# Optimization experiments

Measured on AMD Instinct MI355X. Metric: run time of the kernel, lower is better.

## Reference

```python
import jax, jax.numpy as jnp
import numpy as np

B, C, H, NH = 4, 512, 768, 12        # docs, seq len, hidden, attn heads
NE, MM = 20, 23                      # entities/doc, max mentions/entity
NP_ = NE * (NE - 1)                  # 380 head-tail pairs per doc
QS, POS, EMB, BLK, NB = 128, 128, 768, 64, 12
NCLS = 97
NEG = -10000.0

def _lin(k, i, o):
    return jax.random.normal(k, (i, o), jnp.float32) / np.sqrt(i)

def setup_inputs():
    key = jax.random.key(0)
    ks = jax.random.split(key, 24)
    seq = jax.random.normal(ks[0], (B, C, H), jnp.float32)
    att = jax.random.uniform(ks[1], (B, NH, C, C), jnp.float32)
    midx = jax.random.randint(ks[2], (B, NE, MM), 0, C)
    cnt = jax.random.randint(ks[3], (B, NE), 1, MM + 1)
    mmask = (jnp.arange(MM)[None, None, :] < cnt[:, :, None]).astype(jnp.float32)
    hh, tt = jnp.meshgrid(jnp.arange(NE), jnp.arange(NE), indexing='ij')
    off = ~jnp.eye(NE, dtype=bool)
    hts = jnp.stack([hh[off], tt[off]], -1)
    hts = jnp.broadcast_to(hts[None], (B, NP_, 2))
    vis = (jax.random.uniform(ks[4], (B, NP_, NP_)) > 0.3).astype(jnp.float32)
    inp = dict(sequence_output=seq, attention=att, mention_idx=midx,
               mention_mask=mmask, hts=hts, visible_mask=vis)
    wspec = [('Wcq', H, QS), ('Weq', H, QS), ('Whe', 2 * H, EMB), ('Wte', 2 * H, EMB),
             ('Wbl', EMB * BLK, EMB), ('Wpp', EMB + 2 * POS, EMB),
             ('Wgq', EMB, EMB), ('Wgk', EMB, EMB), ('Wgv', EMB, EMB),
             ('Wp1', 3 * EMB, EMB), ('Wp2', EMB, NCLS)]
    for j, (nm, i, o) in enumerate(wspec):
        inp[nm] = _lin(ks[5 + j], i, o)
        inp['b' + nm[1:]] = jnp.zeros((o,), jnp.float32)
    for nm in ('bgq', 'bgk', 'bgv'):
        inp.pop(nm)
    inp['pos_emb'] = jax.random.normal(ks[20], (42, POS), jnp.float32) * 0.02
    return inp

def reference(sequence_output, attention, mention_idx, mention_mask, hts, visible_mask,
              Wcq, bcq, Weq, beq, Whe, bhe, Wte, bte, Wbl, bbl, Wpp, bpp,
              Wgq, Wgk, Wgv, Wp1, bp1, Wp2, bp2, pos_emb):
    b3 = jnp.arange(B)[:, None, None]
    # per-entity mention gather (padded mentions zeroed, as in the torch loop)
    ent_emb = sequence_output[b3, mention_idx] * mention_mask[..., None]        # [B,NE,MM,H]
    att_t = jnp.transpose(attention, (0, 2, 1, 3))                              # [B,C,NH,C]
    ent_att = att_t[b3, mention_idx] * mention_mask[..., None, None]            # [B,NE,MM,NH,C]
    cnt = mention_mask.sum(-1)[..., None, None]
    ent_att = ent_att.sum(2) / cnt                                              # mean over valid mentions [B,NE,NH,C]

    bi = jnp.arange(B)[:, None]
    hi, ti = hts[..., 0], hts[..., 1]
    hs_m, ts_m = ent_emb[bi, hi], ent_emb[bi, ti]                               # [B,P,MM,H]
    hmask, tmask = mention_mask[bi, hi], mention_mask[bi, ti]                   # [B,P,MM]
    ht_att = (ent_att[bi, hi] * ent_att[bi, ti]).mean(2)                        # mean over heads [B,P,C]
    ht_att = ht_att / (ht_att.sum(-1, keepdims=True) + 1e-5)
    rs = jnp.einsum('bld,bpl->bpd', sequence_output, ht_att)                    # context [B,P,H]

    htq = rs @ Wcq + bcq                                                        # [B,P,QS]
    scale = 1.0 / np.sqrt(EMB)                                                  # original divides by sqrt(emb_size)
    G1 = jnp.einsum('bpq,bpmq->bpm', htq, hs_m @ Weq + beq) * scale
    G2 = jnp.einsum('bpq,bpmq->bpm', htq, ts_m @ Weq + beq) * scale
    G1 = jnp.where(hmask > 0, G1, NEG)
    G2 = jnp.where(tmask > 0, G2, NEG)
    hs = jnp.einsum('bpm,bpmh->bph', jax.nn.softmax(G1, -1), hs_m)
    ts = jnp.einsum('bpm,bpmh->bph', jax.nn.softmax(G2, -1), ts_m)

    hs = jnp.tanh(jnp.concatenate([hs, rs], -1) @ Whe + bhe)                    # [B,P,EMB]
    ts = jnp.tanh(jnp.concatenate([ts, rs], -1) @ Wte + bte)
    bh = hs.reshape(B, NP_, NB, BLK)
    bt = ts.reshape(B, NP_, NB, BLK)
    pair = (bh[..., :, None] * bt[..., None, :]).reshape(B, NP_, EMB * BLK)     # grouped bilinear feature
    pair = pair @ Wbl + bbl                                                     # [B,P,EMB]
    hs_core, ts_core = pos_emb[hi], pos_emb[ti]                                 # [B,P,POS]
    pair = jnp.tanh(jnp.concatenate([hs_core, pair, ts_core], -1) @ Wpp + bpp)

    # pair graph: one masked self-attention layer over pairs with residual
    q, k, v = pair @ Wgq, pair @ Wgk, pair @ Wgv
    sc = jnp.einsum('bpd,bqd->bpq', q, k) / np.sqrt(EMB)
    sc = jnp.where(visible_mask > 0, sc, NEG)
    pair = pair + jnp.einsum('bpq,bqd->bpd', jax.nn.softmax(sc, -1), v)

    feat = jnp.concatenate([hs, ts, pair], -1)                                  # [B,P,3*EMB]
    logits = jnp.tanh(feat @ Wp1 + bp1) @ Wp2 + bp2                             # dropout is identity at eval
    return logits.reshape(B * NP_, NCLS)
```

## Files before the change

### kernel.cpp

```cpp
#include <hip/hip_runtime.h>
#include <hip/hip_bf16.h>

#define Bn   4
#define Cn   512
#define Hn   768
#define NHn  12
#define NEn  20
#define MMn  23
#define Pn   380
#define Mr   1520
#define QSn  128
#define NEGV (-10000.0f)
#define SCL  0.036084391824351615f

typedef unsigned int uint32;
typedef __attribute__((ext_vector_type(4))) float float4v;
typedef __attribute__((ext_vector_type(2))) _Float16 half2v;
typedef __attribute__((ext_vector_type(2))) __fp16 fp16x2;
typedef __attribute__((ext_vector_type(8))) _Float16 half8;

__device__ __forceinline__ unsigned short f2h(float f){
    return __builtin_bit_cast(unsigned short, (_Float16)f);
}
__device__ __forceinline__ uint32 pkrtz(float a, float b){
    fp16x2 h = __builtin_amdgcn_cvt_pkrtz(a, b);
    return __builtin_bit_cast(uint32, h);
}
__device__ __forceinline__ half8 mulsplat(half8 a, uint32 hd){
    half2v s = __builtin_bit_cast(half2v, hd);
    union { half8 h; half2v c[4]; } u, v;
    u.h = a;
    #pragma unroll
    for (int i = 0; i < 4; i++) v.c[i] = u.c[i] * s;
    return v.h;
}
__device__ __forceinline__ void gl_lds16(const unsigned short* g, unsigned short* l){
    __builtin_amdgcn_global_load_lds(
        (const __attribute__((address_space(1))) void*)g,
        (__attribute__((address_space(3))) void*)l, 16, 0, 0);
}

static const size_t o_HS = 0;
static const size_t o_TS = 1167360;
static const size_t o_PB = 2334720;
static const size_t Xo   = 3502080;
static const size_t oEA = Xo;
static const size_t oEE = Xo+491520;
static const size_t oEK = Xo+1904640;
static const size_t oHA = Xo+2140160;
static const size_t oHQ = Xo+2918400;
static const size_t oSH = Xo+3112960;
static const size_t oST = Xo+4280320;
static const size_t oRS = Xo+5447680;
static const size_t oSEQT = Xo+6615040;
static const size_t oWCQ = Xo;
static const size_t oWEQ = Xo+49152;
static const size_t oWHE = Xo;
static const size_t oWTE = Xo+589824;
static const size_t oWBL = Xo;
static const size_t oFP = Xo;
static const size_t oPT = Xo+1556480;
static const size_t oQ  = Xo+2723840;
static const size_t oKT = Xo+3891200;
static const size_t oV  = Xo+5058560;
static const size_t oP2 = Xo+6225920;
static const size_t oT1 = Xo+7393280;
static const size_t oWPP = Xo+8560640;
static const size_t oWGQ = Xo+8953856;
static const size_t oWGK = Xo+9248768;
static const size_t oWGV = Xo+9543680;
static const size_t oWP1 = Xo+9838592;
static const size_t oWP2 = Xo+10723328;


__global__ __launch_bounds__(256) void k_ent_att(const float* __restrict__ att,
    const int* __restrict__ midx, const float* __restrict__ mmask, float* __restrict__ ea)
{
    int x = blockIdx.x;
    int nh = x % NHn; int e = (x / NHn) % NEn; int b = x / (NHn * NEn);
    __shared__ int   sidx[MMn];
    __shared__ float smsk[MMn];
    int t = threadIdx.x;
    if (t < MMn) { sidx[t] = midx[(b*NEn+e)*MMn + t]; smsk[t] = mmask[(b*NEn+e)*MMn + t]; }
    __syncthreads();
    float cnt = 0.f;
    for (int m = 0; m < MMn; m++) cnt += smsk[m];
    for (int c = t; c < Cn; c += 256) {
        float acc = 0.f;
        for (int m = 0; m < MMn; m++)
            acc += smsk[m] * att[((size_t)(b*NHn+nh)*Cn + sidx[m])*Cn + c];
        ea[(size_t)x*Cn + c] = acc / cnt;
    }
}

__global__ __launch_bounds__(256) void k_ent_emb(const float* __restrict__ seq,
    const int* __restrict__ midx, const float* __restrict__ mmask, float* __restrict__ ee)
{
    int x = blockIdx.x;
    int b = x / (NEn*MMn);
    int idx = midx[x]; float msk = mmask[x];
    int t = threadIdx.x;
    for (int h = t; h < Hn; h += 256)
        ee[(size_t)x*Hn + h] = msk * seq[((size_t)b*Cn + idx)*Hn + h];
}

__global__ __launch_bounds__(256) void k_htatt(const float* __restrict__ ea,
    const int* __restrict__ hts, float* __restrict__ hta)
{
    int row = blockIdx.x; int b = row / Pn;
    int he = hts[row*2], te = hts[row*2+1];
    __shared__ float sc[Cn];
    __shared__ float red[256];
    int t = threadIdx.x;
    const float* eah = ea + (size_t)(b*NEn+he)*NHn*Cn;
    const float* eat = ea + (size_t)(b*NEn+te)*NHn*Cn;
    for (int c = t; c < Cn; c += 256) {
        float a = 0.f;
        for (int nh = 0; nh < NHn; nh++) a += eah[nh*Cn+c]*eat[nh*Cn+c];
        sc[c] = a * (1.0f/NHn);
    }
    __syncthreads();
    float ps = sc[t] + sc[t+256];
    red[t] = ps; __syncthreads();
    for (int s = 128; s > 0; s >>= 1) { if (t < s) red[t] += red[t+s]; __syncthreads(); }
    float inv = 1.0f/(red[0] + 1e-5f);
    for (int c = t; c < Cn; c += 256) hta[(size_t)row*Cn + c] = sc[c]*inv;
}

__global__ __launch_bounds__(256) void k_select(const float* __restrict__ htq,
    const float* __restrict__ ekey, const float* __restrict__ ee,
    const float* __restrict__ mmask, const int* __restrict__ hts,
    float* __restrict__ selh, float* __restrict__ selt)
{
    int row = blockIdx.x; int side = blockIdx.y;
    int b = row / Pn;
    int e = hts[row*2 + side];
    __shared__ float qv[QSn];
    __shared__ float gsc[MMn];
    __shared__ float ew[MMn];
    int t = threadIdx.x;
    if (t < QSn) qv[t] = htq[(size_t)row*QSn + t];
    __syncthreads();
    if (t < MMn) {
        const float* kr = ekey + ((size_t)(b*NEn+e)*MMn + t)*QSn;
        float g = 0.f;
        for (int qq = 0; qq < QSn; qq++) g += qv[qq]*kr[qq];
        g *= SCL;
        float msk = mmask[(b*NEn+e)*MMn + t];
        gsc[t] = (msk > 0.f) ? g : NEGV;
    }
    __syncthreads();
    float mx = -1e30f;
    for (int m = 0; m < MMn; m++) mx = fmaxf(mx, gsc[m]);
    if (t < MMn) ew[t] = expf(gsc[t] - mx);
    __syncthreads();
    float s = 0.f;
    for (int m = 0; m < MMn; m++) s += ew[m];
    float invs = 1.0f/s;
    float* dst = side ? selt : selh;
    const float* eb = ee + (size_t)(b*NEn+e)*MMn*Hn;
    for (int h = t; h < Hn; h += 256) {
        float o = 0.f;
        for (int m = 0; m < MMn; m++) o += ew[m]*eb[(size_t)m*Hn + h];
        dst[(size_t)row*Hn + h] = o*invs;
    }
}

struct WD { const float* src; unsigned short* dst; int K; int N; int Npad; int t0; };
struct WT8 { WD d[8]; int nd; };

__global__ __launch_bounds__(256) void k_wtr(WT8 tab)
{
    int b = blockIdx.x;
    int i = 0;
    while (i+1 < tab.nd && b >= tab.d[i+1].t0) i++;
    WD d = tab.d[i];
    int tile = b - d.t0;
    int ktiles = d.K >> 6;
    int kt = tile % ktiles, nt = tile / ktiles;
    int k0 = kt*64, n0 = nt*64;
    __shared__ __align__(16) unsigned short tl[64][72];
    int t = threadIdx.x;
    int nl = t & 63, rq = t >> 6;
    #pragma unroll
    for (int r = 0; r < 16; r++) {
        int kl = r*4 + rq;
        float v = (n0+nl < d.N) ? d.src[(size_t)(k0+kl)*d.N + n0 + nl] : 0.f;
        tl[nl][kl] = f2h(v);
    }
    __syncthreads();
    int nn2 = t >> 2, kk0 = (t & 3) * 16;
    uint4 a = *(const uint4*)&tl[nn2][kk0];
    uint4 bq = *(const uint4*)&tl[nn2][kk0+8];
    uint4* dst = (uint4*)&d.dst[(size_t)(n0+nn2)*d.K + k0 + kk0];
    dst[0] = a; dst[1] = bq;
}

template<int MODE, int TM>
__global__ __launch_bounds__(256,4) void k_gmfma(
    const float* __restrict__ A0, const float* __restrict__ A1, const float* __restrict__ A2,
    int KA, int KB, int KC,
    const unsigned short* __restrict__ Wt,
    const float* __restrict__ bias, float* __restrict__ out,
    float* __restrict__ out2, float* __restrict__ out3,
    int Mtot, int N, int kchunk,
    long aStride, long wStride, long oStride)
{
    __shared__ __align__(16) unsigned short sa[64][72];
    __shared__ __align__(16) unsigned short sw[64][72];
    int t = threadIdx.x;
    int K = KA + KB + KC;
    int row0 = blockIdx.x * 64;
    int n0 = blockIdx.y * 64;
    int bz = blockIdx.z;
    const float* Ab = A0; const unsigned short* W = Wt; float* O = out;
    if (MODE & 32) { Ab += (size_t)bz*aStride; W += (size_t)bz*wStride; O += (size_t)bz*oStride; }
    int k0 = 0, k1 = K;
    if (MODE & 1) { k0 = bz*kchunk; k1 = k0 + kchunk; }
    int lane = t & 63, w = t >> 6, ln = lane & 15, q = lane >> 4;
    int sr = t >> 2;
    int sk = (t & 3) * 16;
    int rA = row0 + sr; if (rA > Mtot-1) rA = Mtot-1;

    float4v acc[4];
    #pragma unroll
    for (int mt = 0; mt < 4; mt++) acc[mt] = (float4v)0.f;

    for (int kk = k0; kk < k1; kk += 64) {
        const float* src; int kloc, Kl, seg;
        if (kk < KA)            { src = Ab; kloc = kk;          Kl = KA; seg = 0; }
        else if (kk < KA + KB)  { src = A1; kloc = kk - KA;     Kl = KB; seg = 1; }
        else                    { src = A2; kloc = kk - KA - KB; Kl = KC; seg = 2; }
        const float* ap = &src[(size_t)rA*Kl + kloc + sk];
        float4 v0 = ((const float4*)ap)[0];
        float4 v1 = ((const float4*)ap)[1];
        float4 v2 = ((const float4*)ap)[2];
        float4 v3 = ((const float4*)ap)[3];
        if (TM && ((TM >> seg) & 1)) {
            v0.x = tanhf(v0.x); v0.y = tanhf(v0.y); v0.z = tanhf(v0.z); v0.w = tanhf(v0.w);
            v1.x = tanhf(v1.x); v1.y = tanhf(v1.y); v1.z = tanhf(v1.z); v1.w = tanhf(v1.w);
            v2.x = tanhf(v2.x); v2.y = tanhf(v2.y); v2.z = tanhf(v2.z); v2.w = tanhf(v2.w);
            v3.x = tanhf(v3.x); v3.y = tanhf(v3.y); v3.z = tanhf(v3.z); v3.w = tanhf(v3.w);
        }
        const uint4* gw = (const uint4*)&W[(size_t)(n0+sr)*K + kk + sk];
        uint4 w0 = gw[0], w1 = gw[1];
        uint4 pa, pb;
        pa.x = pkrtz(v0.x, v0.y); pa.y = pkrtz(v0.z, v0.w);
        pa.z = pkrtz(v1.x, v1.y); pa.w = pkrtz(v1.z, v1.w);
        pb.x = pkrtz(v2.x, v2.y); pb.y = pkrtz(v2.z, v2.w);
        pb.z = pkrtz(v3.x, v3.y); pb.w = pkrtz(v3.z, v3.w);
        *(uint4*)&sa[sr][sk]   = pa;
        *(uint4*)&sa[sr][sk+8] = pb;
        *(uint4*)&sw[sr][sk]   = w0;
        *(uint4*)&sw[sr][sk+8] = w1;
        __syncthreads();
        half8 b0 = *(const half8*)&sw[w*16+ln][q*8];
        half8 b1 = *(const half8*)&sw[w*16+ln][32 + q*8];
        #pragma unroll
        for (int mt = 0; mt < 4; mt++) {
            half8 a0 = *(const half8*)&sa[mt*16+ln][q*8];
            half8 a1 = *(const half8*)&sa[mt*16+ln][32 + q*8];
            acc[mt] = __builtin_amdgcn_mfma_f32_16x16x32_f16(a0, b0, acc[mt], 0, 0, 0);
            acc[mt] = __builtin_amdgcn_mfma_f32_16x16x32_f16(a1, b1, acc[mt], 0, 0, 0);
        }
        __syncthreads();
    }
    int nn = n0 + w*16 + ln;
    if (MODE & 16) {
        int sg = nn / Hn; int nl = nn - sg*Hn;
        #pragma unroll
        for (int mt = 0; mt < 4; mt++) {
            #pragma unroll
            for (int r = 0; r < 4; r++) {
                int row = row0 + mt*16 + q*4 + r;
                if (row >= Mtot) continue;
                float val = acc[mt][r];
                if (sg == 0)      out [(size_t)row*Hn + nl] = val;
                else if (sg == 2) out3[(size_t)row*Hn + nl] = val;
                else {
                    int bb = row / Pn, pp = row % Pn;
                    out2[((size_t)bb*Hn + nl)*Pn + pp] = val;
                }
            }
        }
        return;
    }
    if (nn >= N) return;
    float bv = (MODE & 4) ? bias[nn] : 0.f;
    #pragma unroll
    for (int mt = 0; mt < 4; mt++) {
        #pragma unroll
        for (int r = 0; r < 4; r++) {
            int row = row0 + mt*16 + q*4 + r;
            if (row >= Mtot) continue;
            float val = acc[mt][r];
            if (MODE & 1) atomicAdd(&O[(size_t)row*N + nn], val);
            else          O[(size_t)row*N + nn] = val + bv;
        }
    }
}

__global__ __launch_bounds__(256) void k_binit(const float* __restrict__ bias,
    float* __restrict__ o, int N)
{
    int idx = blockIdx.x*256 + threadIdx.x;
    o[idx] = bias[idx % N];
}

__global__ __launch_bounds__(256) void k_binit3(const float* __restrict__ b0,
    const float* __restrict__ b1, const float* __restrict__ b2, float* __restrict__ o)
{
    int idx = blockIdx.x*256 + threadIdx.x;
    int r = idx / (Mr*Hn);
    const float* bb = (r == 0) ? b0 : ((r == 1) ? b1 : b2);
    o[idx] = bb[idx % Hn];
}

__global__ __launch_bounds__(256,3) void k_blmfma(const float* __restrict__ hs,
    const float* __restrict__ ts, const unsigned short* __restrict__ Wt,
    float* __restrict__ pb)
{
    __shared__ __align__(16) unsigned short hsl[2][64][64];
    __shared__ __align__(16) unsigned short tsl[2][64][64];
    __shared__ __align__(16) unsigned short wbuf[2][64][64];
    int t = threadIdx.x;
    int bid = blockIdx.x + 24*(blockIdx.y + 12*(int)blockIdx.z);
    int sb = (bid & 7)*216 + (bid >> 3);
    int p_t = sb % 24; int r2 = sb / 24;
    int p0 = p_t * 64;
    int d0 = (r2 % 12) * 64;
    int g  = r2 / 12;
    int lane = t & 63, w = t >> 6, ln = lane & 15, q = lane >> 4;
    int xr = (ln & 7) << 3;

    const unsigned short* Wd = Wt + (size_t)d0*49152;
    auto stage = [&](int cc, int bufi){
        int n2 = 2*g + (cc >> 6);
        size_t kb = (size_t)n2*4096 + (size_t)(cc & 63)*64;
        #pragma unroll
        for (int pass = 0; pass < 2; pass++) {
            int r = pass*32 + (t >> 3);
            int c0s = (t & 7) * 8;
            gl_lds16(Wd + (size_t)r*49152 + kb + (c0s ^ ((r & 7) << 3)),
                     &wbuf[bufi][r][c0s]);
        }
    };
    stage(0, 0);

    {
        int p = t & 63; int s = t >> 6;
        int nn = s >> 1; int c0 = (s & 1) * 32;
        int xw = (p & 7) << 3;
        int pr = p0 + p; if (pr > Mr-1) pr = Mr-1;
        int n = 2*g + nn;
        const float* hp = hs + (size_t)pr*Hn + n*64 + c0;
        const float* tp = ts + (size_t)pr*Hn + n*64 + c0;
        #pragma unroll
        for (int b2 = 0; b2 < 2; b2++) {
            const float4* hp4 = (const float4*)(hp + b2*16);
            const float4* tp4 = (const float4*)(tp + b2*16);
            float4 x0=hp4[0], x1=hp4[1], x2=hp4[2], x3=hp4[3];
            uint4 oh, oh2;
            oh.x = pkrtz(tanhf(x0.x),tanhf(x0.y)); oh.y = pkrtz(tanhf(x0.z),tanhf(x0.w));
            oh.z = pkrtz(tanhf(x1.x),tanhf(x1.y)); oh.w = pkrtz(tanhf(x1.z),tanhf(x1.w));
            oh2.x = pkrtz(tanhf(x2.x),tanhf(x2.y)); oh2.y = pkrtz(tanhf(x2.z),tanhf(x2.w));
            oh2.z = pkrtz(tanhf(x3.x),tanhf(x3.y)); oh2.w = pkrtz(tanhf(x3.z),tanhf(x3.w));
            *(uint4*)&hsl[nn][p][(c0 + b2*16)     ^ xw] = oh;
            *(uint4*)&hsl[nn][p][(c0 + b2*16 + 8) ^ xw] = oh2;
            float4 y0=tp4[0], y1=tp4[1], y2=tp4[2], y3=tp4[3];
            uint4 ot, ot2;
            ot.x = pkrtz(tanhf(y0.x),tanhf(y0.y)); ot.y = pkrtz(tanhf(y0.z),tanhf(y0.w));
            ot.z = pkrtz(tanhf(y1.x),tanhf(y1.y)); ot.w = pkrtz(tanhf(y1.z),tanhf(y1.w));
            ot2.x = pkrtz(tanhf(y2.x),tanhf(y2.y)); ot2.y = pkrtz(tanhf(y2.z),tanhf(y2.w));
            ot2.z = pkrtz(tanhf(y3.x),tanhf(y3.y)); ot2.w = pkrtz(tanhf(y3.z),tanhf(y3.w));
            *(uint4*)&tsl[nn][p][(c0 + b2*16)     ^ xw] = ot;
            *(uint4*)&tsl[nn][p][(c0 + b2*16 + 8) ^ xw] = ot2;
        }
    }
    __syncthreads();

    float4v acc[4];
    #pragma unroll
    for (int e = 0; e < 4; e++) acc[e] = (float4v)0.f;

    int buf = 0;
    #pragma unroll
    for (int nn = 0; nn < 2; nn++) {
        half8 tsr0[4], tsr1[4];
        #pragma unroll
        for (int e = 0; e < 4; e++) {
            tsr0[e] = *(const half8*)&tsl[nn][e*16+ln][(q*8) ^ xr];
            tsr1[e] = *(const half8*)&tsl[nn][e*16+ln][(32 + q*8) ^ xr];
        }
        for (int ci = 0; ci < 64; ci++) {
            int cc = nn*64 + ci;
            if (cc + 1 < 128) stage(cc+1, buf^1);
            uint32 hd[4];
            #pragma unroll
            for (int e = 0; e < 4; e++) {
                uint32 hv = hsl[nn][e*16+ln][ci ^ xr];
                hd[e] = __builtin_amdgcn_perm(hv, hv, 0x01000100u);
            }
            #pragma unroll
            for (int c = 0; c < 2; c++) {
                half8 wf = *(const half8*)&wbuf[buf][w*16+ln][(c*32 + q*8) ^ xr];
                #pragma unroll
                for (int e = 0; e < 4; e++) {
                    half8 bfr = mulsplat(c ? tsr1[e] : tsr0[e], hd[e]);
                    acc[e] = __builtin_amdgcn_mfma_f32_16x16x32_f16(wf, bfr, acc[e], 0, 0, 0);
                }
            }
            __syncthreads();
            buf ^= 1;
        }
    }
    #pragma unroll
    for (int e = 0; e < 4; e++) {
        int p = p0 + e*16 + ln;
        if (p >= Mr) continue;
        int dbase = d0 + w*16 + q*4;
        #pragma unroll
        for (int r = 0; r < 4; r++)
            atomicAdd(&pb[(size_t)p*Hn + dbase + r], acc[e][r]);
    }
}


__global__ __launch_bounds__(256) void k_featpp(const float* __restrict__ pairbl,
    const float* __restrict__ pos, const int* __restrict__ hts, float* __restrict__ fpp)
{
    int row = blockIdx.x; int t = threadIdx.x;
    int he = hts[row*2], te = hts[row*2+1];
    float* dst = fpp + (size_t)row*1024;
    if (t < 128) { dst[t] = pos[he*128 + t]; dst[896 + t] = pos[te*128 + t]; }
    for (int h = t; h < Hn; h += 256) dst[128 + h] = pairbl[(size_t)row*Hn + h];
}

__global__ __launch_bounds__(256) void k_graph(const float* __restrict__ q,
    const float* __restrict__ kT, const float* __restrict__ v, const float* __restrict__ vis,
    const float* __restrict__ pairT, float* __restrict__ pair2)
{
    int row = blockIdx.x; int b = row / Pn; int p = row % Pn;
    __shared__ float qs[Hn];
    __shared__ float sc[Pn];
    __shared__ float red[256];
    int t = threadIdx.x;
    for (int h = t; h < Hn; h += 256) qs[h] = q[(size_t)row*Hn + h];
    __syncthreads();
    for (int qq = t; qq < Pn; qq += 256) {
        const float* kcol = kT + (size_t)b*Hn*Pn + qq;
        float a = 0.f;
        for (int h = 0; h < Hn; h++) a += qs[h]*kcol[(size_t)h*Pn];
        a *= SCL;
        float ms = vis[((size_t)b*Pn + p)*Pn + qq];
        sc[qq] = (ms > 0.f) ? a : NEGV;
    }
    __syncthreads();
    float mx = -1e30f;
    for (int qq = t; qq < Pn; qq += 256) mx = fmaxf(mx, sc[qq]);
    red[t] = mx; __syncthreads();
    for (int s = 128; s > 0; s >>= 1) { if (t < s) red[t] = fmaxf(red[t], red[t+s]); __syncthreads(); }
    mx = red[0];
    __syncthreads();
    float ps = 0.f;
    for (int qq = t; qq < Pn; qq += 256) { float e2 = expf(sc[qq]-mx); sc[qq] = e2; ps += e2; }
    red[t] = ps; __syncthreads();
    for (int s = 128; s > 0; s >>= 1) { if (t < s) red[t] += red[t+s]; __syncthreads(); }
    float invs = 1.0f/red[0];
    __syncthreads();
    float a0 = 0.f, a1 = 0.f, a2 = 0.f;
    for (int qq = 0; qq < Pn; qq++) {
        float sv = sc[qq];
        const float* vr = v + ((size_t)b*Pn+qq)*Hn + t;
        a0 += sv*vr[0]; a1 += sv*vr[256]; a2 += sv*vr[512];
    }
    const float* pt = pairT + (size_t)row*Hn + t;
    float* o = pair2 + (size_t)row*Hn + t;
    o[0]   = tanhf(pt[0])   + a0*invs;
    o[256] = tanhf(pt[256]) + a1*invs;
    o[512] = tanhf(pt[512]) + a2*invs;
}

__global__ __launch_bounds__(256) void k_fillu(unsigned int* p, unsigned int v, int n){
    int i = blockIdx.x*256 + threadIdx.x;
    if (i < n) p[i] = v;
}

extern "C" void kernel_launch(void* const* d_in, const int* in_sizes, int n_in,
                              void* d_out, int out_size, void* d_ws, size_t ws_size,
                              hipStream_t stream)
{
    const float* seq  = (const float*)d_in[0];
    const float* att  = (const float*)d_in[1];
    const int*   midx = (const int*)d_in[2];
    const float* mmask= (const float*)d_in[3];
    const int*   hts  = (const int*)d_in[4];
    const float* vis  = (const float*)d_in[5];
    const float* Wcq = (const float*)d_in[6];  const float* bcq = (const float*)d_in[7];
    const float* Weq = (const float*)d_in[8];  const float* beq = (const float*)d_in[9];
    const float* Whe = (const float*)d_in[10]; const float* bhe = (const float*)d_in[11];
    const float* Wte = (const float*)d_in[12]; const float* bte = (const float*)d_in[13];
    const float* Wbl = (const float*)d_in[14]; const float* bbl = (const float*)d_in[15];
    const float* Wpp = (const float*)d_in[16]; const float* bpp = (const float*)d_in[17];
    const float* Wgq = (const float*)d_in[18];
    const float* Wgk = (const float*)d_in[19];
    const float* Wgv = (const float*)d_in[20];
    const float* Wp1 = (const float*)d_in[21]; const float* bp1 = (const float*)d_in[22];
    const float* Wp2 = (const float*)d_in[23]; const float* bp2 = (const float*)d_in[24];
    const float* pos = (const float*)d_in[25];
    float* ws = (float*)d_ws;
    float* out = (float*)d_out;
    const float* nul = nullptr;
    float* nulw = nullptr;

    if (ws_size < 89505792ULL) {
        int n = out_size/2;
        k_fillu<<<(n+255)/256, 256, 0, stream>>>((unsigned int*)d_out, 0x476A476Au, n);
        return;
    }

    unsigned short* WCQt = (unsigned short*)(ws + oWCQ);
    unsigned short* WEQt = (unsigned short*)(ws + oWEQ);
    unsigned short* SEQt = (unsigned short*)(ws + oSEQT);
    unsigned short* WHEt = (unsigned short*)(ws + oWHE);
    unsigned short* WTEt = (unsigned short*)(ws + oWTE);
    unsigned short* WBLt = (unsigned short*)(ws + oWBL);
    unsigned short* WPPt = (unsigned short*)(ws + oWPP);
    unsigned short* WGQt = (unsigned short*)(ws + oWGQ);
    unsigned short* WP1t = (unsigned short*)(ws + oWP1);
    unsigned short* WP2t = (unsigned short*)(ws + oWP2);

    k_ent_att<<<Bn*NEn*NHn, 256, 0, stream>>>(att, midx, mmask, ws + oEA);
    k_ent_emb<<<Bn*NEn*MMn, 256, 0, stream>>>(seq, midx, mmask, ws + oEE);
    k_htatt<<<Mr, 256, 0, stream>>>(ws + oEA, hts, ws + oHA);

    {
        WT8 tb{}; tb.nd = 6;
        tb.d[0] = { Wcq, WCQt, 768, 128, 128, 0 };
        tb.d[1] = { Weq, WEQt, 768, 128, 128, 24 };
        for (int b = 0; b < 4; b++)
            tb.d[2+b] = { seq + (size_t)b*Cn*Hn, SEQt + (size_t)b*Hn*Cn, Cn, Hn, Hn, 48 + b*96 };
        k_wtr<<<432, 256, 0, stream>>>(tb);
    }
    k_gmfma<32,0><<<dim3(6,12,4), 256, 0, stream>>>(ws + oHA, nul, nul, Cn, 0, 0,
        SEQt, nul, ws + oRS, nulw, nulw, Pn, Hn, 0,
        (long)Pn*Cn, (long)Hn*Cn, (long)Pn*Hn);
    k_gmfma<4,0><<<dim3(24,2,1), 256, 0, stream>>>(ws + oRS, nul, nul, Hn, 0, 0,
        WCQt, bcq, ws + oHQ, nulw, nulw, Mr, QSn, 0, 0, 0, 0);
    k_gmfma<4,0><<<dim3(29,2,1), 256, 0, stream>>>(ws + oEE, nul, nul, Hn, 0, 0,
        WEQt, beq, ws + oEK, nulw, nulw, Bn*NEn*MMn, QSn, 0, 0, 0, 0);
    k_select<<<dim3(Mr,2), 256, 0, stream>>>(ws + oHQ, ws + oEK, ws + oEE,
        mmask, hts, ws + oSH, ws + oST);

    {
        WT8 tb{}; tb.nd = 2;
        tb.d[0] = { Whe, WHEt, 1536, 768, 768, 0 };
        tb.d[1] = { Wte, WTEt, 1536, 768, 768, 288 };
        k_wtr<<<576, 256, 0, stream>>>(tb);
    }
    k_binit3<<<(3*Mr*Hn)/256, 256, 0, stream>>>(bhe, bte, bbl, ws + o_HS);
    k_gmfma<1,0><<<dim3(24,12,3), 256, 0, stream>>>(ws + oSH, ws + oRS, nul, Hn, Hn, 0,
        WHEt, nul, ws + o_HS, nulw, nulw, Mr, Hn, 512, 0, 0, 0);
    k_gmfma<1,0><<<dim3(24,12,3), 256, 0, stream>>>(ws + oST, ws + oRS, nul, Hn, Hn, 0,
        WTEt, nul, ws + o_TS, nulw, nulw, Mr, Hn, 512, 0, 0, 0);

    {
        WT8 tb{}; tb.nd = 1;
        tb.d[0] = { Wbl, WBLt, 49152, 768, 768, 0 };
        k_wtr<<<9216, 256, 0, stream>>>(tb);
    }
    k_blmfma<<<dim3(24,12,6), 256, 0, stream>>>(ws + o_HS, ws + o_TS, WBLt, ws + o_PB);

    k_featpp<<<Mr, 256, 0, stream>>>(ws + o_PB, pos, hts, ws + oFP);

    {
        WT8 tb{}; tb.nd = 6;
        tb.d[0] = { Wpp, WPPt, 1024, 768, 768, 0 };
        tb.d[1] = { Wgq, WGQt, 768, 768, 768, 192 };
        tb.d[2] = { Wgk, (unsigned short*)(ws + oWGK), 768, 768, 768, 336 };
        tb.d[3] = { Wgv, (unsigned short*)(ws + oWGV), 768, 768, 768, 480 };
        tb.d[4] = { Wp1, WP1t, 2304, 768, 768, 624 };
        tb.d[5] = { Wp2, WP2t, 768, 97, 128, 1056 };
        k_wtr<<<1080, 256, 0, stream>>>(tb);
    }
    k_binit<<<(Mr*Hn)/256, 256, 0, stream>>>(bpp, ws + oPT, Hn);
    k_gmfma<1,0><<<dim3(24,12,2), 256, 0, stream>>>(ws + oFP, nul, nul, 1024, 0, 0,
        WPPt, nul, ws + oPT, nulw, nulw, Mr, Hn, 512, 0, 0, 0);
    k_gmfma<16,1><<<dim3(24,36,1), 256, 0, stream>>>(ws + oPT, nul, nul, Hn, 0, 0,
        WGQt, nul, ws + oQ, ws + oKT, ws + oV, Mr, 3*Hn, 0, 0, 0, 0);
    k_graph<<<Mr, 256, 0, stream>>>(ws + oQ, ws + oKT, ws + oV, vis, ws + oPT, ws + oP2);
    k_binit<<<(Mr*Hn)/256, 256, 0, stream>>>(bp1, ws + oT1, Hn);
    k_gmfma<1,3><<<dim3(24,12,3), 256, 0, stream>>>(ws + o_HS, ws + o_TS, ws + oP2,
        Hn, Hn, Hn, WP1t, nul, ws + oT1, nulw, nulw, Mr, Hn, 768, 0, 0, 0);
    k_gmfma<4,1><<<dim3(24,2,1), 256, 0, stream>>>(ws + oT1, nul, nul, Hn, 0, 0,
        WP2t, bp2, out, nulw, nulw, Mr, 97, 0, 0, 0, 0);
}
```

Measured before the change: 1.024 ms.

## Replace scalar pair-graph attention with MFMA GEMMs plus separate softmax

The fused per-row scalar attention kernel is split into three steps. An MFMA batched GEMM computes the QK^T scores, a row softmax kernel applies the visibility mask and writes padded probabilities, and a second MFMA GEMM multiplies them by a transposed fp16 V, followed by a residual tanh-add kernel. The QKV projection epilogue now writes K and transposed V in fp16 with a 384-padded stride, which adds a zero-fill launch and reduces precision. The goal is to move the O(P^2·H) attention work from scalar FMAs with strided loads onto matrix cores, at the cost of more launches and intermediate round trips through memory.

```diff
diff --git a/kernel.cpp b/kernel.cpp
--- a/kernel.cpp
+++ b/kernel.cpp
@@ -62,6 +62,7 @@
 static const size_t oPT = Xo+1556480;
 static const size_t oQ  = Xo+2723840;
 static const size_t oKT = Xo+3891200;
+static const size_t oP_ = oKT+583680;
 static const size_t oV  = Xo+5058560;
 static const size_t oP2 = Xo+6225920;
 static const size_t oT1 = Xo+7393280;
@@ -276,10 +277,10 @@
                 if (row >= Mtot) continue;
                 float val = acc[mt][r];
                 if (sg == 0)      out [(size_t)row*Hn + nl] = val;
-                else if (sg == 2) out3[(size_t)row*Hn + nl] = val;
+                else if (sg == 1) ((unsigned short*)out2)[(size_t)row*Hn + nl] = f2h(val);
                 else {
                     int bb = row / Pn, pp = row % Pn;
-                    out2[((size_t)bb*Hn + nl)*Pn + pp] = val;
+                    ((unsigned short*)out3)[((size_t)bb*Hn + nl)*384 + pp] = f2h(val);
                 }
             }
         }
@@ -436,49 +437,39 @@
     for (int h = t; h < Hn; h += 256) dst[128 + h] = pairbl[(size_t)row*Hn + h];
 }
 
-__global__ __launch_bounds__(256) void k_graph(const float* __restrict__ q,
-    const float* __restrict__ kT, const float* __restrict__ v, const float* __restrict__ vis,
-    const float* __restrict__ pairT, float* __restrict__ pair2)
+__global__ __launch_bounds__(256) void k_smax(const float* __restrict__ S,
+    const float* __restrict__ vis, float* __restrict__ P)
 {
     int row = blockIdx.x; int b = row / Pn; int p = row % Pn;
-    __shared__ float qs[Hn];
     __shared__ float sc[Pn];
     __shared__ float red[256];
     int t = threadIdx.x;
-    for (int h = t; h < Hn; h += 256) qs[h] = q[(size_t)row*Hn + h];
-    __syncthreads();
+    const float* Sr = S + (size_t)b*Pn*Pn + (size_t)p*Pn;
+    const float* vr = vis + ((size_t)b*Pn + p)*Pn;
+    float mx0 = -1e30f;
     for (int qq = t; qq < Pn; qq += 256) {
-        const float* kcol = kT + (size_t)b*Hn*Pn + qq;
-        float a = 0.f;
-        for (int h = 0; h < Hn; h++) a += qs[h]*kcol[(size_t)h*Pn];
-        a *= SCL;
-        float ms = vis[((size_t)b*Pn + p)*Pn + qq];
-        sc[qq] = (ms > 0.f) ? a : NEGV;
-    }
-    __syncthreads();
-    float mx = -1e30f;
-    for (int qq = t; qq < Pn; qq += 256) mx = fmaxf(mx, sc[qq]);
-    red[t] = mx; __syncthreads();
+        float a = Sr[qq] * SCL;
+        a = (vr[qq] > 0.f) ? a : NEGV;
+        sc[qq] = a; mx0 = fmaxf(mx0, a);
+    }
+    red[t] = mx0; __syncthreads();
     for (int s = 128; s > 0; s >>= 1) { if (t < s) red[t] = fmaxf(red[t], red[t+s]); __syncthreads(); }
-    mx = red[0];
-    __syncthreads();
+    float mx = red[0]; __syncthreads();
     float ps = 0.f;
-    for (int qq = t; qq < Pn; qq += 256) { float e2 = expf(sc[qq]-mx); sc[qq] = e2; ps += e2; }
+    for (int qq = t; qq < Pn; qq += 256) { float e = expf(sc[qq]-mx); sc[qq] = e; ps += e; }
     red[t] = ps; __syncthreads();
     for (int s = 128; s > 0; s >>= 1) { if (t < s) red[t] += red[t+s]; __syncthreads(); }
-    float invs = 1.0f/red[0];
-    __syncthreads();
-    float a0 = 0.f, a1 = 0.f, a2 = 0.f;
-    for (int qq = 0; qq < Pn; qq++) {
-        float sv = sc[qq];
-        const float* vr = v + ((size_t)b*Pn+qq)*Hn + t;
-        a0 += sv*vr[0]; a1 += sv*vr[256]; a2 += sv*vr[512];
-    }
-    const float* pt = pairT + (size_t)row*Hn + t;
-    float* o = pair2 + (size_t)row*Hn + t;
-    o[0]   = tanhf(pt[0])   + a0*invs;
-    o[256] = tanhf(pt[256]) + a1*invs;
-    o[512] = tanhf(pt[512]) + a2*invs;
+    float inv = 1.0f/red[0];
+    __syncthreads();
+    float* Pr = P + (size_t)b*Pn*384 + (size_t)p*384;
+    for (int qq = t; qq < Pn; qq += 256) Pr[qq] = sc[qq]*inv;
+    if (t < 4) Pr[Pn + t] = 0.f;
+}
+
+__global__ __launch_bounds__(256) void k_resid(const float* __restrict__ pt, float* __restrict__ p2)
+{
+    size_t i = (size_t)blockIdx.x*256 + threadIdx.x;
+    p2[i] = tanhf(pt[i]) + p2[i];
 }
 
 __global__ __launch_bounds__(256) void k_fillu(unsigned int* p, unsigned int v, int n){
@@ -529,6 +520,8 @@
     unsigned short* WGQt = (unsigned short*)(ws + oWGQ);
     unsigned short* WP1t = (unsigned short*)(ws + oWP1);
     unsigned short* WP2t = (unsigned short*)(ws + oWP2);
+    unsigned short* K16  = (unsigned short*)(ws + oKT);
+    unsigned short* Vt16 = (unsigned short*)(ws + oV);
 
     k_ent_att<<<Bn*NEn*NHn, 256, 0, stream>>>(att, midx, mmask, ws + oEA);
     k_ent_emb<<<Bn*NEn*MMn, 256, 0, stream>>>(seq, midx, mmask, ws + oEE);
@@ -586,9 +579,17 @@
     k_binit<<<(Mr*Hn)/256, 256, 0, stream>>>(bpp, ws + oPT, Hn);
     k_gmfma<1,0><<<dim3(24,12,2), 256, 0, stream>>>(ws + oFP, nul, nul, 1024, 0, 0,
         WPPt, nul, ws + oPT, nulw, nulw, Mr, Hn, 512, 0, 0, 0);
+    k_fillu<<<2304, 256, 0, stream>>>((unsigned int*)Vt16, 0u, Bn*Hn*384/2);
     k_gmfma<16,1><<<dim3(24,36,1), 256, 0, stream>>>(ws + oPT, nul, nul, Hn, 0, 0,
-        WGQt, nul, ws + oQ, ws + oKT, ws + oV, Mr, 3*Hn, 0, 0, 0, 0);
-    k_graph<<<Mr, 256, 0, stream>>>(ws + oQ, ws + oKT, ws + oV, vis, ws + oPT, ws + oP2);
+        WGQt, nul, ws + oQ, (float*)K16, (float*)Vt16, Mr, 3*Hn, 0, 0, 0, 0);
+    k_gmfma<32,0><<<dim3(6,6,4), 256, 0, stream>>>(ws + oQ, nul, nul, Hn, 0, 0,
+        K16, nul, ws + oP2, nulw, nulw, Pn, Pn, 0,
+        (long)Pn*Hn, (long)Pn*Hn, (long)Pn*Pn);
+    k_smax<<<Mr, 256, 0, stream>>>(ws + oP2, vis, ws + oP_);
+    k_gmfma<32,0><<<dim3(6,12,4), 256, 0, stream>>>(ws + oP_, nul, nul, 384, 0, 0,
+        Vt16, nul, ws + oP2, nulw, nulw, Pn, Hn, 0,
+        (long)Pn*384, (long)Hn*384, (long)Pn*Hn);
+    k_resid<<<(Mr*Hn)/256, 256, 0, stream>>>(ws + oPT, ws + oP2);
     k_binit<<<(Mr*Hn)/256, 256, 0, stream>>>(bp1, ws + oT1, Hn);
     k_gmfma<1,3><<<dim3(24,12,3), 256, 0, stream>>>(ws + o_HS, ws + o_TS, ws + oP2,
         Hn, Hn, Hn, WP1t, nul, ws + oT1, nulw, nulw, Mr, Hn, 768, 0, 0, 0);
```

Measured after the change: 908.3 us. -11.3%, faster.
